# Kernel optimization log

Measured on AMD Instinct MI355X. Metric: run time of the kernel, lower is better.

The kernel has to match this reference:

```python
import jax, jax.numpy as jnp
import numpy as np

N_NODES = 100000
N_EDGES = 3200000
IN_Z = 32
PROJ_H = 64
LOOP_D = 32
DEC_H = 64


def setup_inputs() -> dict:
    key = jax.random.key(0)
    ks = jax.random.split(key, 10)
    z_mod = jax.random.normal(ks[0], (N_NODES, IN_Z), dtype=jnp.float32)
    edge_index = jax.random.randint(ks[1], (2, N_EDGES), 0, N_NODES, dtype=jnp.int64)
    # loop_proj: Linear(32->64), ReLU, Linear(64->32)
    w1 = jax.random.normal(ks[2], (IN_Z, PROJ_H), dtype=jnp.float32) / np.sqrt(IN_Z)
    b1 = jnp.zeros((PROJ_H,), dtype=jnp.float32)
    w2 = jax.random.normal(ks[3], (PROJ_H, LOOP_D), dtype=jnp.float32) / np.sqrt(PROJ_H)
    b2 = jnp.zeros((LOOP_D,), dtype=jnp.float32)
    # decoder: Linear(2*loop_dim -> dec_hidden), ReLU, Linear(dec_hidden -> 1)
    dw1 = jax.random.normal(ks[4], (2 * LOOP_D, DEC_H), dtype=jnp.float32) / np.sqrt(2 * LOOP_D)
    db1 = jnp.zeros((DEC_H,), dtype=jnp.float32)
    dw2 = jax.random.normal(ks[5], (DEC_H, 1), dtype=jnp.float32) / np.sqrt(DEC_H)
    db2 = jnp.zeros((1,), dtype=jnp.float32)
    return {"z_mod": z_mod, "edge_index": edge_index, "w1": w1, "b1": b1,
            "w2": w2, "b2": b2, "dw1": dw1, "db1": db1, "dw2": dw2, "db2": db2}


def reference(z_mod, edge_index, w1, b1, w2, b2, dw1, db1, dw2, db2):
    # loop_proj: z_mod -> z_loop  [N, loop_dim]
    h = jax.nn.relu(z_mod @ w1 + b1)
    z_loop = h @ w2 + b2
    # edge-wise decoder: gather, concat, MLP
    zi = z_loop[edge_index[0]]            # [E, loop_dim]
    zj = z_loop[edge_index[1]]            # [E, loop_dim]
    he = jnp.concatenate([zi, zj], axis=-1)  # [E, 2*loop_dim]
    he = jax.nn.relu(he @ dw1 + db1)         # [E, dec_hidden]
    logits = (he @ dw2 + db2)[..., 0]        # [E]
    return logits
```

## Files before the change

kernel.cpp:

```cpp
#include <hip/hip_runtime.h>


typedef short bfrag4 __attribute__((ext_vector_type(4)));
typedef float f32x4v __attribute__((ext_vector_type(4)));
typedef int   i32x4  __attribute__((ext_vector_type(4)));

#define N_NODES 100000
#define N_EDGES 3200000

__device__ __forceinline__ unsigned short f2bf(float f) {
    unsigned int i = __float_as_uint(f);
    unsigned int r = i + 0x7FFFu + ((i >> 16) & 1u);
    return (unsigned short)(r >> 16);
}

__device__ __forceinline__ float bf2f(unsigned short b) {
    unsigned int u = ((unsigned int)b) << 16;
    return __uint_as_float(u);
}

__device__ __forceinline__ bfrag4 cvt4(float x0, float x1, float x2, float x3) {
    bfrag4 v;
    v[0] = (short)f2bf(x0);
    v[1] = (short)f2bf(x1);
    v[2] = (short)f2bf(x2);
    v[3] = (short)f2bf(x3);
    return v;
}

__global__ __launch_bounds__(256) void node_proj_kernel(
    const float* __restrict__ z_mod,
    const float* __restrict__ w1,
    const float* __restrict__ b1,
    const float* __restrict__ w2,
    const float* __restrict__ b2,
    unsigned short* __restrict__ z16,
    unsigned int*   __restrict__ gmax)
{
    __shared__ unsigned short hbuf[4][16 * 72];

    const int tid  = threadIdx.x;
    const int wave = tid >> 6;
    const int lane = tid & 63;
    const int quad = lane >> 4;
    const int col  = lane & 15;

    bfrag4 bw1[2][4];
    float  bias1[4];
    for (int t = 0; t < 4; ++t) {
        const int n = col + 16 * t;
        for (int s = 0; s < 2; ++s)
            for (int j = 0; j < 4; ++j)
                bw1[s][t][j] = (short)f2bf(w1[(s * 16 + quad * 4 + j) * 64 + n]);
        bias1[t] = b1[n];
    }
    bfrag4 bw2[4][2];
    float  bias2[2];
    for (int t = 0; t < 2; ++t) {
        const int n = col + 16 * t;
        for (int s = 0; s < 4; ++s)
            for (int j = 0; j < 4; ++j)
                bw2[s][t][j] = (short)f2bf(w2[(s * 16 + quad * 4 + j) * 32 + n]);
        bias2[t] = b2[n];
    }

    unsigned short* hrow = &hbuf[wave][0];

    const int gwave  = blockIdx.x * 4 + wave;
    const int nwaves = gridDim.x * 4;
    const int ntiles = N_NODES / 16;

    float wmax = 0.f;

    for (int tile = gwave; tile < ntiles; tile += nwaves) {
        const int node0 = tile * 16;
        const float* zrow = z_mod + (size_t)(node0 + col) * 32;

        f32x4v za0 = *(const f32x4v*)(zrow + 0 * 16 + quad * 4);
        f32x4v za1 = *(const f32x4v*)(zrow + 1 * 16 + quad * 4);
        bfrag4 a10 = cvt4(za0[0], za0[1], za0[2], za0[3]);
        bfrag4 a11 = cvt4(za1[0], za1[1], za1[2], za1[3]);

        f32x4v acc[4];
        for (int t = 0; t < 4; ++t) {
            f32x4v c = {bias1[t], bias1[t], bias1[t], bias1[t]};
            c = __builtin_amdgcn_mfma_f32_16x16x16bf16_1k(a10, bw1[0][t], c, 0, 0, 0);
            c = __builtin_amdgcn_mfma_f32_16x16x16bf16_1k(a11, bw1[1][t], c, 0, 0, 0);
            acc[t] = c;
        }

        for (int t = 0; t < 4; ++t)
            for (int r = 0; r < 4; ++r) {
                float v = acc[t][r];
                v = v > 0.f ? v : 0.f;
                hrow[(quad * 4 + r) * 72 + (col + 16 * t)] = f2bf(v);
            }
        asm volatile("" ::: "memory");

        f32x4v acc2[2];
        for (int t = 0; t < 2; ++t)
            acc2[t] = (f32x4v){bias2[t], bias2[t], bias2[t], bias2[t]};
        for (int s = 0; s < 4; ++s) {
            bfrag4 a2 = *(const bfrag4*)(hrow + col * 72 + s * 16 + quad * 4);
            for (int t = 0; t < 2; ++t)
                acc2[t] = __builtin_amdgcn_mfma_f32_16x16x16bf16_1k(a2, bw2[s][t], acc2[t], 0, 0, 0);
        }
        asm volatile("" ::: "memory");

        for (int t = 0; t < 2; ++t)
            for (int r = 0; r < 4; ++r) {
                float v = acc2[t][r];
                wmax = fmaxf(wmax, fabsf(v));
                z16[(size_t)(node0 + quad * 4 + r) * 32 + (col + 16 * t)] =
                    f2bf(v);
            }
    }

    for (int mask = 1; mask <= 32; mask <<= 1)
        wmax = fmaxf(wmax, __shfl_xor(wmax, mask, 64));
    if (lane == 0)
        atomicMax(gmax, __float_as_uint(wmax));
}

__global__ __launch_bounds__(256) void quant8_kernel(
    const unsigned short* __restrict__ z16,
    const unsigned int*   __restrict__ gmax,
    char* __restrict__ z8)
{
    const int idx = blockIdx.x * 256 + threadIdx.x;
    if (idx >= N_NODES * 32 / 8) return;
    const float M   = __uint_as_float(*gmax);
    const float inv = 127.f / fmaxf(M, 1e-30f);

    i32x4 v = *(const i32x4*)(z16 + (size_t)idx * 8);
    unsigned long long pk = 0;
#pragma unroll
    for (int i = 0; i < 4; ++i) {
        unsigned int w = (unsigned int)v[i];
        int q0 = (int)rintf(bf2f((unsigned short)(w & 0xFFFF)) * inv);
        int q1 = (int)rintf(bf2f((unsigned short)(w >> 16)) * inv);
        pk |= ((unsigned long long)(q0 & 0xFF)) << (16 * i);
        pk |= ((unsigned long long)(q1 & 0xFF)) << (16 * i + 8);
    }
    *(unsigned long long*)(z8 + (size_t)idx * 8) = pk;
}

__global__ __launch_bounds__(256) void edge_dec_kernel(
    const int*          __restrict__ eidx,
    const char*         __restrict__ z8,
    const unsigned int* __restrict__ gmax,
    const float*        __restrict__ dw1,
    const float*        __restrict__ db1,
    const float*        __restrict__ dw2,
    const float*        __restrict__ db2,
    float* __restrict__ out)
{
    const int tid  = threadIdx.x;
    const int lane = tid & 63;
    const int quad = lane >> 4;
    const int col  = lane & 15;
    const int ss   = quad >> 1;
    const int hf   = quad & 1;

    const float gz = __uint_as_float(*gmax) * (1.f / 127.f);

    i32x4 awq[4];
    float wscv[4];
    for (int mt = 0; mt < 4; ++mt) {
        const int m = 16 * mt + col;
        float w[16];
        float mx = 0.f;
        for (int j = 0; j < 16; ++j) {
            w[j] = dw1[(quad * 16 + j) * 64 + m];
            mx = fmaxf(mx, fabsf(w[j]));
        }
        mx = fmaxf(mx, __shfl_xor(mx, 16, 64));
        mx = fmaxf(mx, __shfl_xor(mx, 32, 64));
        wscv[mt] = mx * (1.f / 127.f);
        const float winv = 127.f / fmaxf(mx, 1e-30f);
        i32x4 a;
        for (int rr = 0; rr < 4; ++rr) {
            int pk = 0;
            for (int bi = 0; bi < 4; ++bi) {
                int q = (int)rintf(w[rr * 4 + bi] * winv);
                pk |= (q & 0xFF) << (8 * bi);
            }
            a[rr] = pk;
        }
        awq[mt] = a;
    }
    float bS[4][4], wS[4][4];
    for (int mt = 0; mt < 4; ++mt)
        for (int r = 0; r < 4; ++r) {
            const float S = __shfl(wscv[mt], quad * 4 + r, 64) * gz;
            bS[mt][r] = db1[16 * mt + quad * 4 + r] / S;
            wS[mt][r] = dw2[16 * mt + quad * 4 + r] * S;
        }
    const float bias2 = db2[0];

    const int gwave  = blockIdx.x * 4 + (tid >> 6);
    const int nwaves = gridDim.x * 4;
    const int npairs = N_EDGES / 32;

    const int iofs = ss * N_EDGES + col;

    int iA = eidx[gwave * 32 + iofs];
    int iB = eidx[gwave * 32 + 16 + iofs];

    for (int p = gwave; p < npairs; p += nwaves) {
        const int e0 = p * 32;

        i32x4 gA = *(const i32x4*)(z8 + (size_t)iA * 32 + hf * 16);
        i32x4 gB = *(const i32x4*)(z8 + (size_t)iB * 32 + hf * 16);

        const int pn = p + nwaves;
        const int pc = pn < npairs ? pn : gwave;
        iA = eidx[pc * 32 + iofs];
        iB = eidx[pc * 32 + 16 + iofs];

        const i32x4 zc = {0, 0, 0, 0};
        i32x4 aA[4], aB[4];
        for (int mt = 0; mt < 4; ++mt) {
            aA[mt] = __builtin_amdgcn_mfma_i32_16x16x64_i8(awq[mt], gA, zc, 0, 0, 0);
            aB[mt] = __builtin_amdgcn_mfma_i32_16x16x64_i8(awq[mt], gB, zc, 0, 0, 0);
        }

        float pA = 0.f, pB = 0.f;
        for (int mt = 0; mt < 4; ++mt)
            for (int r = 0; r < 4; ++r) {
                float hA = (float)aA[mt][r] + bS[mt][r];
                float hB = (float)aB[mt][r] + bS[mt][r];
                hA = hA > 0.f ? hA : 0.f;
                hB = hB > 0.f ? hB : 0.f;
                pA = fmaf(hA, wS[mt][r], pA);
                pB = fmaf(hB, wS[mt][r], pB);
            }
        pA += __shfl_xor(pA, 16, 64);
        pA += __shfl_xor(pA, 32, 64);
        pB += __shfl_xor(pB, 16, 64);
        pB += __shfl_xor(pB, 32, 64);

        if (lane < 32) {
            float v = (lane < 16 ? pA : pB) + bias2;
            out[e0 + lane] = v;
        }
    }
}

extern "C" void kernel_launch(void* const* d_in, const int* in_sizes, int n_in,
                              void* d_out, int out_size, void* d_ws, size_t ws_size,
                              hipStream_t stream) {
    const float* z_mod = (const float*)d_in[0];
    const int*   eidx  = (const int*)d_in[1];
    const float* w1    = (const float*)d_in[2];
    const float* b1    = (const float*)d_in[3];
    const float* w2    = (const float*)d_in[4];
    const float* b2    = (const float*)d_in[5];
    const float* dw1   = (const float*)d_in[6];
    const float* db1   = (const float*)d_in[7];
    const float* dw2   = (const float*)d_in[8];
    const float* db2   = (const float*)d_in[9];
    float* out = (float*)d_out;

    char*         z8   = (char*)d_ws;
    unsigned int* gmax = (unsigned int*)((char*)d_ws + (size_t)N_NODES * 32);
    unsigned short* z16 = (unsigned short*)d_out;

    hipMemsetAsync(gmax, 0, 4, stream);
    node_proj_kernel<<<512, 256, 0, stream>>>(z_mod, w1, b1, w2, b2, z16, gmax);
    quant8_kernel<<<1563, 256, 0, stream>>>(z16, gmax, z8);
    edge_dec_kernel<<<2048, 256, 0, stream>>>(eidx, z8, gmax, dw1, db1, dw2, db2, out);
}
```

Before: 171.9 us.

## Fuse int8 quantization into node projection via grid barrier; nontemporal edge I/O

The separate quantization kernel is folded into the node projection kernel. A software grid-wide barrier (an atomic counter plus spin-wait) makes every block wait until the global max is final, and then the blocks quantize the bf16 projections to int8 in a grid-stride loop. This removes one kernel launch and its gap. It relies on all 512 blocks being co-resident, otherwise the spin-wait deadlocks. Separately, the edge index loads and output stores in the decoder now use nontemporal hints to reduce cache pollution from the streamed data.

```diff
diff --git a/kernel.cpp b/kernel.cpp
--- a/kernel.cpp
+++ b/kernel.cpp
@@ -7,6 +7,7 @@
 
 #define N_NODES 100000
 #define N_EDGES 3200000
+#define NODE_BLOCKS 512
 
 __device__ __forceinline__ unsigned short f2bf(float f) {
     unsigned int i = __float_as_uint(f);
@@ -35,7 +36,8 @@
     const float* __restrict__ w2,
     const float* __restrict__ b2,
     unsigned short* __restrict__ z16,
-    unsigned int*   __restrict__ gmax)
+    char*           __restrict__ z8,
+    unsigned int*   __restrict__ gc)
 {
     __shared__ unsigned short hbuf[4][16 * 72];
 
@@ -119,36 +121,43 @@
     for (int mask = 1; mask <= 32; mask <<= 1)
         wmax = fmaxf(wmax, __shfl_xor(wmax, mask, 64));
     if (lane == 0)
-        atomicMax(gmax, __float_as_uint(wmax));
-}
-
-__global__ __launch_bounds__(256) void quant8_kernel(
-    const unsigned short* __restrict__ z16,
-    const unsigned int*   __restrict__ gmax,
-    char* __restrict__ z8)
-{
-    const int idx = blockIdx.x * 256 + threadIdx.x;
-    if (idx >= N_NODES * 32 / 8) return;
-    const float M   = __uint_as_float(*gmax);
+        atomicMax(&gc[0], __float_as_uint(wmax));
+
+    __threadfence();
+    __syncthreads();
+    if (tid == 0) {
+        __hip_atomic_fetch_add(&gc[1], 1u, __ATOMIC_ACQ_REL,
+                               __HIP_MEMORY_SCOPE_AGENT);
+        while (__hip_atomic_load(&gc[1], __ATOMIC_ACQUIRE,
+                                 __HIP_MEMORY_SCOPE_AGENT) < NODE_BLOCKS)
+            __builtin_amdgcn_s_sleep(8);
+    }
+    __syncthreads();
+    __threadfence();
+
+    const float M = __uint_as_float(
+        __hip_atomic_load(&gc[0], __ATOMIC_RELAXED, __HIP_MEMORY_SCOPE_AGENT));
     const float inv = 127.f / fmaxf(M, 1e-30f);
-
-    i32x4 v = *(const i32x4*)(z16 + (size_t)idx * 8);
-    unsigned long long pk = 0;
+    for (int idx = blockIdx.x * 256 + tid; idx < N_NODES * 32 / 8;
+         idx += NODE_BLOCKS * 256) {
+        i32x4 v = *(const i32x4*)(z16 + (size_t)idx * 8);
+        unsigned long long pk = 0;
 #pragma unroll
-    for (int i = 0; i < 4; ++i) {
-        unsigned int w = (unsigned int)v[i];
-        int q0 = (int)rintf(bf2f((unsigned short)(w & 0xFFFF)) * inv);
-        int q1 = (int)rintf(bf2f((unsigned short)(w >> 16)) * inv);
-        pk |= ((unsigned long long)(q0 & 0xFF)) << (16 * i);
-        pk |= ((unsigned long long)(q1 & 0xFF)) << (16 * i + 8);
-    }
-    *(unsigned long long*)(z8 + (size_t)idx * 8) = pk;
+        for (int i = 0; i < 4; ++i) {
+            unsigned int w = (unsigned int)v[i];
+            int q0 = (int)rintf(bf2f((unsigned short)(w & 0xFFFF)) * inv);
+            int q1 = (int)rintf(bf2f((unsigned short)(w >> 16)) * inv);
+            pk |= ((unsigned long long)(q0 & 0xFF)) << (16 * i);
+            pk |= ((unsigned long long)(q1 & 0xFF)) << (16 * i + 8);
+        }
+        *(unsigned long long*)(z8 + (size_t)idx * 8) = pk;
+    }
 }
 
 __global__ __launch_bounds__(256) void edge_dec_kernel(
     const int*          __restrict__ eidx,
     const char*         __restrict__ z8,
-    const unsigned int* __restrict__ gmax,
+    const unsigned int* __restrict__ gc,
     const float*        __restrict__ dw1,
     const float*        __restrict__ db1,
     const float*        __restrict__ dw2,
@@ -162,7 +171,7 @@
     const int ss   = quad >> 1;
     const int hf   = quad & 1;
 
-    const float gz = __uint_as_float(*gmax) * (1.f / 127.f);
+    const float gz = __uint_as_float(gc[0]) * (1.f / 127.f);
 
     i32x4 awq[4];
     float wscv[4];
@@ -204,8 +213,8 @@
 
     const int iofs = ss * N_EDGES + col;
 
-    int iA = eidx[gwave * 32 + iofs];
-    int iB = eidx[gwave * 32 + 16 + iofs];
+    int iA = __builtin_nontemporal_load(eidx + gwave * 32 + iofs);
+    int iB = __builtin_nontemporal_load(eidx + gwave * 32 + 16 + iofs);
 
     for (int p = gwave; p < npairs; p += nwaves) {
         const int e0 = p * 32;
@@ -215,8 +224,8 @@
 
         const int pn = p + nwaves;
         const int pc = pn < npairs ? pn : gwave;
-        iA = eidx[pc * 32 + iofs];
-        iB = eidx[pc * 32 + 16 + iofs];
+        iA = __builtin_nontemporal_load(eidx + pc * 32 + iofs);
+        iB = __builtin_nontemporal_load(eidx + pc * 32 + 16 + iofs);
 
         const i32x4 zc = {0, 0, 0, 0};
         i32x4 aA[4], aB[4];
@@ -242,7 +251,7 @@
 
         if (lane < 32) {
             float v = (lane < 16 ? pA : pB) + bias2;
-            out[e0 + lane] = v;
+            __builtin_nontemporal_store(v, out + e0 + lane);
         }
     }
 }
@@ -262,12 +271,13 @@
     const float* db2   = (const float*)d_in[9];
     float* out = (float*)d_out;
 
-    char*         z8   = (char*)d_ws;
-    unsigned int* gmax = (unsigned int*)((char*)d_ws + (size_t)N_NODES * 32);
+    char*         z8 = (char*)d_ws;
+    unsigned int* gc = (unsigned int*)((char*)d_ws + (size_t)N_NODES * 32);
     unsigned short* z16 = (unsigned short*)d_out;
 
-    hipMemsetAsync(gmax, 0, 4, stream);
-    node_proj_kernel<<<512, 256, 0, stream>>>(z_mod, w1, b1, w2, b2, z16, gmax);
-    quant8_kernel<<<1563, 256, 0, stream>>>(z16, gmax, z8);
-    edge_dec_kernel<<<2048, 256, 0, stream>>>(eidx, z8, gmax, dw1, db1, dw2, db2, out);
-}
+    hipMemsetAsync(gc, 0, 8, stream);
+    node_proj_kernel<<<NODE_BLOCKS, 256, 0, stream>>>(z_mod, w1, b1, w2, b2,
+                                                      z16, z8, gc);
+    edge_dec_kernel<<<2048, 256, 0, stream>>>(eidx, z8, gc, dw1, db1, dw2,
+                                              db2, out);
+}
```

Measured after the change: 268.1 us. 1.56x slower.
